# Kernel tuning notes

Hardware: AMD Instinct MI355X
Metric: run time of the kernel (lower is better)

Reference implementation:

```python
import jax, jax.numpy as jnp
import numpy as np

B, S, D, H = 2, 2048, 1024, 16
DK = D // H


def setup_inputs() -> dict:
    key = jax.random.key(0)
    ks = jax.random.split(key, 9)
    sc = 0.02
    return {
        "x": jax.random.normal(ks[0], (B, S, D), dtype=jnp.float32),
        "attention_mask": jnp.ones((B, S), dtype=jnp.int32),
        "Wq": jax.random.normal(ks[1], (D, D), dtype=jnp.float32) * sc,
        "bq": jax.random.normal(ks[2], (D,), dtype=jnp.float32) * sc,
        "Wk": jax.random.normal(ks[3], (D, D), dtype=jnp.float32) * sc,
        "bk": jax.random.normal(ks[4], (D,), dtype=jnp.float32) * sc,
        "Wv": jax.random.normal(ks[5], (D, D), dtype=jnp.float32) * sc,
        "bv": jax.random.normal(ks[6], (D,), dtype=jnp.float32) * sc,
        "Wo": jax.random.normal(ks[7], (D, D), dtype=jnp.float32) * sc,
        "bo": jax.random.normal(ks[8], (D,), dtype=jnp.float32) * sc,
    }


def reference(x, attention_mask, Wq, bq, Wk, bk, Wv, bv, Wo, bo):
    b, s, d = x.shape
    # projections (Linear: x @ W + b) then split heads -> [b, h, s, dk]
    def heads(t):
        return t.reshape(b, s, H, DK).transpose(0, 2, 1, 3)
    Q = heads(x @ Wq + bq)
    K = heads(x @ Wk + bk)
    V = heads(x @ Wv + bv)
    # NOTE: original computes K @ Q^T (not Q @ K^T) and applies NO 1/sqrt(dk) scale
    scores = jnp.einsum("bhid,bhjd->bhij", K, Q)  # [b, h, s, s]
    causal = jnp.tril(jnp.ones((s, s), dtype=bool))  # [s, s]
    final_mask = attention_mask[:, None, None, :].astype(bool) & causal[None, None]
    scores = jnp.where(final_mask, scores, -jnp.inf)
    attn = jax.nn.softmax(scores, axis=-1)
    out = jnp.einsum("bhij,bhjd->bhid", attn, V)  # [b, h, s, dk]
    out = out.transpose(0, 2, 1, 3).reshape(b, s, d)
    return out @ Wo + bo
```

## Files before the change

### kernel.cpp

```cpp
#include <hip/hip_runtime.h>
#include <stdint.h>
#include <stddef.h>


typedef short bf16x8 __attribute__((ext_vector_type(8)));
typedef float f32x4  __attribute__((ext_vector_type(4)));

__device__ __forceinline__ short f2bf(float f) {
  union { float f; uint32_t u; } a; a.f = f;
  uint32_t r = a.u + 0x7fffu + ((a.u >> 16) & 1u);
  return (short)(r >> 16);
}
__device__ __forceinline__ float bf2f(short s) {
  union { uint32_t u; float f; } a; a.u = ((uint32_t)(uint16_t)s) << 16;
  return a.f;
}
__device__ __forceinline__ uint32_t pack2bf(float a, float b) {
  union { float f; uint32_t u; } x, y; x.f = a; y.f = b;
  return (x.u >> 16) | (y.u & 0xffff0000u);
}
__device__ __forceinline__ float fast_exp2(float x) {
#if __has_builtin(__builtin_amdgcn_exp2f)
  return __builtin_amdgcn_exp2f(x);
#else
  return exp2f(x);
#endif
}
__device__ __forceinline__ void async16(const void* g, void* l) {
  __builtin_amdgcn_global_load_lds(
      (const __attribute__((address_space(1))) uint32_t*)g,
      (__attribute__((address_space(3))) uint32_t*)l, 16, 0, 0);
}
#define MFMA(a, b, c) __builtin_amdgcn_mfma_f32_16x16x32_bf16((a), (b), (c), 0, 0, 0)

__global__ void k_split_x(const float* __restrict__ x, short* __restrict__ xhi,
                          short* __restrict__ xlo) {
  int i = blockIdx.x * 256 + threadIdx.x;
  float4 v = ((const float4*)x)[i];
  short4 h, l;
  h.x = f2bf(v.x); l.x = f2bf(v.x - bf2f(h.x));
  h.y = f2bf(v.y); l.y = f2bf(v.y - bf2f(h.y));
  h.z = f2bf(v.z); l.z = f2bf(v.z - bf2f(h.z));
  h.w = f2bf(v.w); l.w = f2bf(v.w - bf2f(h.w));
  ((short4*)xhi)[i] = h;
  ((short4*)xlo)[i] = l;
}

__global__ void k_prep_w(const float* __restrict__ Wq, const float* __restrict__ Wk,
                         const float* __restrict__ Wv, const float* __restrict__ Wo,
                         short* __restrict__ whi, short* __restrict__ wo) {
  __shared__ float T[64][65];
  int z = blockIdx.z;
  const float* W = (z == 0) ? Wq : (z == 1) ? Wk : (z == 2) ? Wv : Wo;
  int n0 = blockIdx.x * 64, k0 = blockIdx.y * 64;
  int t = threadIdx.x;
  int rr = t >> 4, cc = (t & 15) * 4;
#pragma unroll
  for (int it = 0; it < 4; ++it) {
    int row = rr + it * 16;
    float4 v = *(const float4*)&W[(size_t)(k0 + row) * 1024 + n0 + cc];
    T[row][cc] = v.x; T[row][cc + 1] = v.y; T[row][cc + 2] = v.z; T[row][cc + 3] = v.w;
  }
  __syncthreads();
  short* oh = (z < 3) ? (whi + (size_t)z * 1048576) : wo;
#pragma unroll
  for (int it = 0; it < 4; ++it) {
    int nrow = rr + it * 16;
    short4 h4;
    h4.x = f2bf(T[cc + 0][nrow]);
    h4.y = f2bf(T[cc + 1][nrow]);
    h4.z = f2bf(T[cc + 2][nrow]);
    h4.w = f2bf(T[cc + 3][nrow]);
    *(short4*)&oh[(size_t)(n0 + nrow) * 1024 + k0 + cc] = h4;
  }
}

__global__ __launch_bounds__(256, 3) void k_gemm_qkv(
    const short* __restrict__ xhi, const short* __restrict__ xlo,
    const short* __restrict__ whi,
    const float* __restrict__ bq, const float* __restrict__ bk,
    const float* __restrict__ bv,
    short* __restrict__ Qhi, short* __restrict__ Qlo,
    short* __restrict__ Khi, short* __restrict__ Klo,
    short* __restrict__ Vt) {
  __shared__ short AH[2][4096];
  __shared__ short AL[2][4096];
  __shared__ short BH[2][4096];
  int tid = threadIdx.x;
  int bx = blockIdx.x;
  int m0 = blockIdx.y * 128;
  int n0g = bx * 128;
  bool SPLIT = (bx < 16);
  int w = tid >> 6, lane = tid & 63, lr = lane & 15, lq = lane >> 4;
  int wm = w >> 1, wn = w & 1;
  f32x4 acc[4][4] = {};

  auto stage = [&](int ks, int pb) {
#pragma unroll
    for (int it = 0; it < 2; ++it) {
      int idx = it * 256 + tid;
      int row = idx >> 2, c = idx & 3;
      int cs = c ^ (row & 3);
      size_t ga = (size_t)(m0 + row) * 1024 + ks * 32 + cs * 8;
      async16(xhi + ga, &AH[pb][idx * 8]);
      if (SPLIT) async16(xlo + ga, &AL[pb][idx * 8]);
      size_t gb = (size_t)(n0g + row) * 1024 + ks * 32 + cs * 8;
      async16(whi + gb, &BH[pb][idx * 8]);
    }
  };

  stage(0, 0);
  int p = 0;
  int g = lq ^ (lr & 3);
  for (int ks = 0; ks < 32; ++ks) {
    __syncthreads();
    if (ks < 31) stage(ks + 1, p ^ 1);
    const bf16x8* A8 = (const bf16x8*)AH[p];
    const bf16x8* L8 = (const bf16x8*)AL[p];
    const bf16x8* B8 = (const bf16x8*)BH[p];
    bf16x8 af[4], al[4], bfr[4];
#pragma unroll
    for (int mt = 0; mt < 4; ++mt) af[mt] = A8[(wm * 64 + mt * 16 + lr) * 4 + g];
#pragma unroll
    for (int nt = 0; nt < 4; ++nt) bfr[nt] = B8[(wn * 64 + nt * 16 + lr) * 4 + g];
    if (SPLIT) {
#pragma unroll
      for (int mt = 0; mt < 4; ++mt) al[mt] = L8[(wm * 64 + mt * 16 + lr) * 4 + g];
    }
#pragma unroll
    for (int mt = 0; mt < 4; ++mt)
#pragma unroll
      for (int nt = 0; nt < 4; ++nt)
        acc[mt][nt] = MFMA(af[mt], bfr[nt], acc[mt][nt]);
    if (SPLIT) {
#pragma unroll
      for (int mt = 0; mt < 4; ++mt)
#pragma unroll
        for (int nt = 0; nt < 4; ++nt)
          acc[mt][nt] = MFMA(al[mt], bfr[nt], acc[mt][nt]);
    }
    p ^= 1;
  }

  int z = bx >> 3;
  const float LOG2E = 1.44269504f;
  if (z == 2) {
#pragma unroll
    for (int nt = 0; nt < 4; ++nt) {
      int dg = (n0g & 1023) + wn * 64 + nt * 16 + lr;
      float bvv = bv[dg];
      int hh = dg >> 6, dk = dg & 63;
#pragma unroll
      for (int mt = 0; mt < 4; ++mt) {
        int row = m0 + wm * 64 + mt * 16 + lq * 4;
        int b_ = row >> 11, s_ = row & 2047;
        short4 pk;
        pk.x = f2bf(acc[mt][nt][0] + bvv);
        pk.y = f2bf(acc[mt][nt][1] + bvv);
        pk.z = f2bf(acc[mt][nt][2] + bvv);
        pk.w = f2bf(acc[mt][nt][3] + bvv);
        *(short4*)&Vt[(size_t)((b_ * 16 + hh) * 64 + dk) * 2048 + s_] = pk;
      }
    }
  } else {
    const float* bias = (z == 0) ? bq : bk;
    short* Ch = (z == 0) ? Qhi : Khi;
    short* Cl = (z == 0) ? Qlo : Klo;
#pragma unroll
    for (int nt = 0; nt < 4; ++nt) {
      int colg = (n0g & 1023) + wn * 64 + nt * 16 + lr;
      float bvv = bias[colg];
#pragma unroll
      for (int mt = 0; mt < 4; ++mt)
#pragma unroll
        for (int r = 0; r < 4; ++r) {
          int row = m0 + wm * 64 + mt * 16 + lq * 4 + r;
          float v = acc[mt][nt][r] + bvv;
          if (z == 0) v *= LOG2E;
          size_t o = (size_t)row * 1024 + colg;
          short hh = f2bf(v);
          Ch[o] = hh;
          Cl[o] = f2bf(v - bf2f(hh));
        }
    }
  }
}

__global__ __launch_bounds__(256, 2) void k_gemm_o(
    const short* __restrict__ Ab, const short* __restrict__ Bb,
    const float* __restrict__ bias, float* __restrict__ Cf) {
  __shared__ short AH[2][4096];
  __shared__ short BH[2][4096];
  int tid = threadIdx.x;
  int m0 = blockIdx.y * 128, n0 = blockIdx.x * 128;
  int w = tid >> 6, lane = tid & 63, lr = lane & 15, lq = lane >> 4;
  int wm = w >> 1, wn = w & 1;
  f32x4 acc[4][4] = {};

  auto stage = [&](int ks, int pb) {
#pragma unroll
    for (int it = 0; it < 2; ++it) {
      int idx = it * 256 + tid;
      int row = idx >> 2, c = idx & 3;
      int cs = c ^ (row & 3);
      async16(Ab + (size_t)(m0 + row) * 1024 + ks * 32 + cs * 8, &AH[pb][idx * 8]);
      async16(Bb + (size_t)(n0 + row) * 1024 + ks * 32 + cs * 8, &BH[pb][idx * 8]);
    }
  };

  stage(0, 0);
  int p = 0;
  int g = lq ^ (lr & 3);
  for (int ks = 0; ks < 32; ++ks) {
    __syncthreads();
    if (ks < 31) stage(ks + 1, p ^ 1);
    const bf16x8* A8 = (const bf16x8*)AH[p];
    const bf16x8* B8 = (const bf16x8*)BH[p];
    bf16x8 af[4], bfr[4];
#pragma unroll
    for (int mt = 0; mt < 4; ++mt) af[mt] = A8[(wm * 64 + mt * 16 + lr) * 4 + g];
#pragma unroll
    for (int nt = 0; nt < 4; ++nt) bfr[nt] = B8[(wn * 64 + nt * 16 + lr) * 4 + g];
#pragma unroll
    for (int mt = 0; mt < 4; ++mt)
#pragma unroll
      for (int nt = 0; nt < 4; ++nt)
        acc[mt][nt] = MFMA(af[mt], bfr[nt], acc[mt][nt]);
    p ^= 1;
  }
#pragma unroll
  for (int nt = 0; nt < 4; ++nt) {
    int col = n0 + wn * 64 + nt * 16 + lr;
    float bvv = bias[col];
#pragma unroll
    for (int mt = 0; mt < 4; ++mt)
#pragma unroll
      for (int r = 0; r < 4; ++r) {
        int row = m0 + wm * 64 + mt * 16 + lq * 4 + r;
        Cf[(size_t)row * 1024 + col] = acc[mt][nt][r] + bvv;
      }
  }
}

__global__ __launch_bounds__(128, 2) void k_attn(
    const short* __restrict__ Khi, const short* __restrict__ Klo,
    const short* __restrict__ Qhi, const short* __restrict__ Qlo,
    const short* __restrict__ Vt, const int* __restrict__ amask,
    short* __restrict__ Obuf) {
  __shared__ short QH[4096];
  __shared__ short QL[4096];
  __shared__ short VS[4096];
  int tid = threadIdx.x;
  int bid = blockIdx.x;
  int xcd = bid & 7, slot = bid >> 3;
  int bh = xcd * 4 + (slot >> 5);
  int p  = slot & 31;
  int b = bh >> 4, h = bh & 15;
  int w = tid >> 6, lane = tid & 63, lr = lane & 15, lq = lane >> 4;
  int bandA = p, bandB = 63 - p;
  int nA = ((p * 32 + 31) >> 6) + 1;

  f32x4 OA[4] = {}, OB[4] = {};
  float lsA = 0.f, lsB = 0.f;
  int baddr0 = (((lq & 1) * 2) * 16 + lr) * 4;
  int baddr1 = baddr0 + 64;

  bf16x8 kh[2], kl[2];
  const bf16x8* Q8 = (const bf16x8*)QH;
  const bf16x8* L8 = (const bf16x8*)QL;
  const bf16x8* V8 = (const bf16x8*)VS;

  for (int t = 0; t < 33; ++t) {
    bool isA = (t < nA);
    int band = isA ? bandA : bandB;
    int jt = isA ? t : t - nA;
    int j0 = jt * 64;
#pragma unroll
    for (int it = 0; it < 4; ++it) {
      int idx = it * 128 + tid;
      int rr = idx >> 3, c = idx & 7;
      int cs = c ^ (rr & 7);
      size_t gq = ((size_t)(b * 2048 + j0 + rr)) * 1024 + h * 64 + cs * 8;
      async16(Qhi + gq, &QH[idx * 8]);
      async16(Qlo + gq, &QL[idx * 8]);
      size_t gv = ((size_t)(bh * 64 + rr)) * 2048 + j0 + cs * 8;
      async16(Vt + gv, &VS[idx * 8]);
    }
    if (t == 0 || t == nA) {
      size_t ra = ((size_t)(b * 2048 + band * 32 + w * 16 + lr)) * 1024 + h * 64;
#pragma unroll
      for (int ks = 0; ks < 2; ++ks) {
        kh[ks] = *(const bf16x8*)(Khi + ra + ks * 32 + lq * 8);
        kl[ks] = *(const bf16x8*)(Klo + ra + ks * 32 + lq * 8);
      }
    }
    __syncthreads();

    int av = amask[b * 2048 + j0 + lane];
    unsigned long long bal = __ballot(av != 0);
    bool allv = (bal == ~0ull);

    f32x4 s[4] = {};
#pragma unroll
    for (int mt = 0; mt < 4; ++mt) {
      int row = mt * 16 + lr;
#pragma unroll
      for (int ks = 0; ks < 2; ++ks) {
        int gi = row * 8 + ((ks * 4 + lq) ^ (row & 7));
        bf16x8 qa = Q8[gi];
        bf16x8 la = L8[gi];
        s[mt] = MFMA(qa, kh[ks], s[mt]);
        s[mt] = MFMA(la, kh[ks], s[mt]);
        s[mt] = MFMA(qa, kl[ks], s[mt]);
      }
    }

    bool diag = (t == nA - 1) || (t == 32);
    int iq = band * 32 + w * 16 + lr;
    float pv[4][4];
#pragma unroll
    for (int mt = 0; mt < 4; ++mt)
#pragma unroll
      for (int r = 0; r < 4; ++r)
        pv[mt][r] = fast_exp2(s[mt][r]);
    if (diag) {
#pragma unroll
      for (int mt = 0; mt < 4; ++mt)
#pragma unroll
        for (int r = 0; r < 4; ++r)
          if (j0 + mt * 16 + lq * 4 + r > iq) pv[mt][r] = 0.f;
    }
    if (!allv) {
#pragma unroll
      for (int mt = 0; mt < 4; ++mt)
#pragma unroll
        for (int r = 0; r < 4; ++r)
          if (!((bal >> (mt * 16 + lq * 4 + r)) & 1)) pv[mt][r] = 0.f;
    }
    uint32_t pd[4][2];
    float lt = 0.f;
#pragma unroll
    for (int mt = 0; mt < 4; ++mt) {
      lt += (pv[mt][0] + pv[mt][1]) + (pv[mt][2] + pv[mt][3]);
      pd[mt][0] = pack2bf(pv[mt][0], pv[mt][1]);
      pd[mt][1] = pack2bf(pv[mt][2], pv[mt][3]);
    }
    if (isA) lsA += lt; else lsB += lt;

    f32x4* O = isA ? OA : OB;
#pragma unroll
    for (int k2 = 0; k2 < 2; ++k2) {
      union { int i[4]; bf16x8 v; } pa;
#pragma unroll
      for (int dd = 0; dd < 4; ++dd) {
        int addr = (dd >> 1) ? baddr1 : baddr0;
        int v0 = __builtin_amdgcn_ds_bpermute(addr, (int)pd[k2 * 2 + 0][dd & 1]);
        int v1 = __builtin_amdgcn_ds_bpermute(addr, (int)pd[k2 * 2 + 1][dd & 1]);
        pa.i[dd] = (lq >> 1) ? v1 : v0;
      }
#pragma unroll
      for (int nt = 0; nt < 4; ++nt) {
        int row = nt * 16 + lr;
        bf16x8 vb = V8[row * 8 + ((k2 * 4 + lq) ^ (row & 7))];
        O[nt] = MFMA(pa.v, vb, O[nt]);
      }
    }
    __syncthreads();
  }

  auto fin = [&](f32x4* O, float ls, int band) {
    float tsum = ls;
    tsum += __shfl_xor(tsum, 16);
    tsum += __shfl_xor(tsum, 32);
    float inv[4];
#pragma unroll
    for (int r = 0; r < 4; ++r) inv[r] = 1.0f / __shfl(tsum, lq * 4 + r, 64);
#pragma unroll
    for (int nt = 0; nt < 4; ++nt)
#pragma unroll
      for (int r = 0; r < 4; ++r) {
        int row = b * 2048 + band * 32 + w * 16 + lq * 4 + r;
        int col = h * 64 + nt * 16 + lr;
        Obuf[(size_t)row * 1024 + col] = f2bf(O[nt][r] * inv[r]);
      }
  };
  fin(OA, lsA, bandA);
  fin(OB, lsB, bandB);
}

extern "C" void kernel_launch(void* const* d_in, const int* in_sizes, int n_in,
                              void* d_out, int out_size, void* d_ws, size_t ws_size,
                              hipStream_t stream) {
  const float* x  = (const float*)d_in[0];
  const int* amask = (const int*)d_in[1];
  const float* Wq = (const float*)d_in[2];
  const float* bq = (const float*)d_in[3];
  const float* Wk = (const float*)d_in[4];
  const float* bk = (const float*)d_in[5];
  const float* Wv = (const float*)d_in[6];
  const float* bv = (const float*)d_in[7];
  const float* Wo = (const float*)d_in[8];
  const float* bo = (const float*)d_in[9];

  char* ws = (char*)d_ws;
  const size_t MB = 1024 * 1024;
  short* xhi = (short*)(ws);
  short* xlo = (short*)(ws + 8 * MB);
  short* whi = (short*)(ws + 16 * MB);
  short* wo  = (short*)(ws + 26 * MB);
  short* Qhi = (short*)(ws + 28 * MB);
  short* Qlo = (short*)(ws + 36 * MB);
  short* Khi = (short*)(ws + 44 * MB);
  short* Klo = (short*)(ws + 52 * MB);
  short* Vt  = (short*)(ws + 60 * MB);
  short* Obuf = xhi;

  k_split_x<<<4096, 256, 0, stream>>>(x, xhi, xlo);
  k_prep_w<<<dim3(16, 16, 4), 256, 0, stream>>>(Wq, Wk, Wv, Wo, whi, wo);

  k_gemm_qkv<<<dim3(24, 32), 256, 0, stream>>>(xhi, xlo, whi, bq, bk, bv,
                                               Qhi, Qlo, Khi, Klo, Vt);
  k_attn<<<1024, 128, 0, stream>>>(Khi, Klo, Qhi, Qlo, Vt, amask, Obuf);
  k_gemm_o<<<dim3(8, 32), 256, 0, stream>>>(Obuf, wo, bo, (float*)d_out);
}
```

Before: 241.7 us.

## Double-buffer attention tiles, 4-warp band pairs, and halve output GEMM tile width

The attention kernel now uses 256 threads, so each block owns two adjacent 32-row query bands, and it double-buffers the Q/V tiles in shared memory. The next tile's async load is issued while the current one is being computed, and one barrier per iteration is dropped. The old pairing of a short band with a long band (33 iterations per block) is replaced by variable-length blocks ordered longest first, which relies on the scheduler to balance the work. The output GEMM switches to 128x64 tiles with more blocks and higher occupancy. In exchange, shared memory per attention block doubles and the work is spread unevenly across blocks.

```diff
diff --git a/kernel.cpp b/kernel.cpp
--- a/kernel.cpp
+++ b/kernel.cpp
@@ -186,16 +186,15 @@
   }
 }
 
-__global__ __launch_bounds__(256, 2) void k_gemm_o(
+__global__ __launch_bounds__(256, 4) void k_gemm_o(
     const short* __restrict__ Ab, const short* __restrict__ Bb,
     const float* __restrict__ bias, float* __restrict__ Cf) {
   __shared__ short AH[2][4096];
-  __shared__ short BH[2][4096];
+  __shared__ short BH[2][2048];
   int tid = threadIdx.x;
-  int m0 = blockIdx.y * 128, n0 = blockIdx.x * 128;
+  int m0 = blockIdx.y * 128, n0 = blockIdx.x * 64;
   int w = tid >> 6, lane = tid & 63, lr = lane & 15, lq = lane >> 4;
-  int wm = w >> 1, wn = w & 1;
-  f32x4 acc[4][4] = {};
+  f32x4 acc[2][4] = {};
 
   auto stage = [&](int ks, int pb) {
 #pragma unroll
@@ -204,6 +203,11 @@
       int row = idx >> 2, c = idx & 3;
       int cs = c ^ (row & 3);
       async16(Ab + (size_t)(m0 + row) * 1024 + ks * 32 + cs * 8, &AH[pb][idx * 8]);
+    }
+    {
+      int idx = tid;
+      int row = idx >> 2, c = idx & 3;
+      int cs = c ^ (row & 3);
       async16(Bb + (size_t)(n0 + row) * 1024 + ks * 32 + cs * 8, &BH[pb][idx * 8]);
     }
   };
@@ -216,13 +220,13 @@
     if (ks < 31) stage(ks + 1, p ^ 1);
     const bf16x8* A8 = (const bf16x8*)AH[p];
     const bf16x8* B8 = (const bf16x8*)BH[p];
-    bf16x8 af[4], bfr[4];
-#pragma unroll
-    for (int mt = 0; mt < 4; ++mt) af[mt] = A8[(wm * 64 + mt * 16 + lr) * 4 + g];
-#pragma unroll
-    for (int nt = 0; nt < 4; ++nt) bfr[nt] = B8[(wn * 64 + nt * 16 + lr) * 4 + g];
-#pragma unroll
-    for (int mt = 0; mt < 4; ++mt)
+    bf16x8 af[2], bfr[4];
+#pragma unroll
+    for (int mt = 0; mt < 2; ++mt) af[mt] = A8[(w * 32 + mt * 16 + lr) * 4 + g];
+#pragma unroll
+    for (int nt = 0; nt < 4; ++nt) bfr[nt] = B8[(nt * 16 + lr) * 4 + g];
+#pragma unroll
+    for (int mt = 0; mt < 2; ++mt)
 #pragma unroll
       for (int nt = 0; nt < 4; ++nt)
         acc[mt][nt] = MFMA(af[mt], bfr[nt], acc[mt][nt]);
@@ -230,71 +234,76 @@
   }
 #pragma unroll
   for (int nt = 0; nt < 4; ++nt) {
-    int col = n0 + wn * 64 + nt * 16 + lr;
+    int col = n0 + nt * 16 + lr;
     float bvv = bias[col];
 #pragma unroll
-    for (int mt = 0; mt < 4; ++mt)
+    for (int mt = 0; mt < 2; ++mt)
 #pragma unroll
       for (int r = 0; r < 4; ++r) {
-        int row = m0 + wm * 64 + mt * 16 + lq * 4 + r;
+        int row = m0 + w * 32 + mt * 16 + lq * 4 + r;
         Cf[(size_t)row * 1024 + col] = acc[mt][nt][r] + bvv;
       }
   }
 }
 
-__global__ __launch_bounds__(128, 2) void k_attn(
+__global__ __launch_bounds__(256, 3) void k_attn(
     const short* __restrict__ Khi, const short* __restrict__ Klo,
     const short* __restrict__ Qhi, const short* __restrict__ Qlo,
     const short* __restrict__ Vt, const int* __restrict__ amask,
     short* __restrict__ Obuf) {
-  __shared__ short QH[4096];
-  __shared__ short QL[4096];
-  __shared__ short VS[4096];
+  __shared__ short QH[2][4096];
+  __shared__ short QL[2][4096];
+  __shared__ short VS[2][4096];
   int tid = threadIdx.x;
   int bid = blockIdx.x;
-  int xcd = bid & 7, slot = bid >> 3;
-  int bh = xcd * 4 + (slot >> 5);
-  int p  = slot & 31;
+  int xcd = bid & 7, idx = bid >> 3;
+  int bh = xcd * 4 + (idx >> 5);
+  int L  = 32 - (idx & 31);
   int b = bh >> 4, h = bh & 15;
   int w = tid >> 6, lane = tid & 63, lr = lane & 15, lq = lane >> 4;
-  int bandA = p, bandB = 63 - p;
-  int nA = ((p * 32 + 31) >> 6) + 1;
-
-  f32x4 OA[4] = {}, OB[4] = {};
-  float lsA = 0.f, lsB = 0.f;
+  int band = 2 * (L - 1) + (w >> 1);
+  int rb0 = band * 32 + (w & 1) * 16;
+
+  bf16x8 kh[2], kl[2];
+  {
+    size_t ra = ((size_t)(b * 2048 + rb0 + lr)) * 1024 + h * 64;
+#pragma unroll
+    for (int ks = 0; ks < 2; ++ks) {
+      kh[ks] = *(const bf16x8*)(Khi + ra + ks * 32 + lq * 8);
+      kl[ks] = *(const bf16x8*)(Klo + ra + ks * 32 + lq * 8);
+    }
+  }
+
+  f32x4 O[4] = {};
+  float ls = 0.f;
+  int iq = rb0 + lr;
   int baddr0 = (((lq & 1) * 2) * 16 + lr) * 4;
   int baddr1 = baddr0 + 64;
 
-  bf16x8 kh[2], kl[2];
-  const bf16x8* Q8 = (const bf16x8*)QH;
-  const bf16x8* L8 = (const bf16x8*)QL;
-  const bf16x8* V8 = (const bf16x8*)VS;
-
-  for (int t = 0; t < 33; ++t) {
-    bool isA = (t < nA);
-    int band = isA ? bandA : bandB;
-    int jt = isA ? t : t - nA;
+  auto stage = [&](int jt, int pb) {
     int j0 = jt * 64;
 #pragma unroll
-    for (int it = 0; it < 4; ++it) {
-      int idx = it * 128 + tid;
-      int rr = idx >> 3, c = idx & 7;
+    for (int it = 0; it < 2; ++it) {
+      int idx2 = it * 256 + tid;
+      int rr = idx2 >> 3, c = idx2 & 7;
       int cs = c ^ (rr & 7);
       size_t gq = ((size_t)(b * 2048 + j0 + rr)) * 1024 + h * 64 + cs * 8;
-      async16(Qhi + gq, &QH[idx * 8]);
-      async16(Qlo + gq, &QL[idx * 8]);
+      async16(Qhi + gq, &QH[pb][idx2 * 8]);
+      async16(Qlo + gq, &QL[pb][idx2 * 8]);
       size_t gv = ((size_t)(bh * 64 + rr)) * 2048 + j0 + cs * 8;
-      async16(Vt + gv, &VS[idx * 8]);
-    }
-    if (t == 0 || t == nA) {
-      size_t ra = ((size_t)(b * 2048 + band * 32 + w * 16 + lr)) * 1024 + h * 64;
-#pragma unroll
-      for (int ks = 0; ks < 2; ++ks) {
-        kh[ks] = *(const bf16x8*)(Khi + ra + ks * 32 + lq * 8);
-        kl[ks] = *(const bf16x8*)(Klo + ra + ks * 32 + lq * 8);
-      }
-    }
+      async16(Vt + gv, &VS[pb][idx2 * 8]);
+    }
+  };
+
+  stage(0, 0);
+  int p = 0;
+  for (int t = 0; t < L; ++t) {
     __syncthreads();
+    if (t + 1 < L) stage(t + 1, p ^ 1);
+    int j0 = t * 64;
+    const bf16x8* Q8 = (const bf16x8*)QH[p];
+    const bf16x8* L8 = (const bf16x8*)QL[p];
+    const bf16x8* V8 = (const bf16x8*)VS[p];
 
     int av = amask[b * 2048 + j0 + lane];
     unsigned long long bal = __ballot(av != 0);
@@ -315,8 +324,7 @@
       }
     }
 
-    bool diag = (t == nA - 1) || (t == 32);
-    int iq = band * 32 + w * 16 + lr;
+    bool diag = (t == L - 1);
     float pv[4][4];
 #pragma unroll
     for (int mt = 0; mt < 4; ++mt)
@@ -338,16 +346,13 @@
           if (!((bal >> (mt * 16 + lq * 4 + r)) & 1)) pv[mt][r] = 0.f;
     }
     uint32_t pd[4][2];
-    float lt = 0.f;
 #pragma unroll
     for (int mt = 0; mt < 4; ++mt) {
-      lt += (pv[mt][0] + pv[mt][1]) + (pv[mt][2] + pv[mt][3]);
+      ls += (pv[mt][0] + pv[mt][1]) + (pv[mt][2] + pv[mt][3]);
       pd[mt][0] = pack2bf(pv[mt][0], pv[mt][1]);
       pd[mt][1] = pack2bf(pv[mt][2], pv[mt][3]);
     }
-    if (isA) lsA += lt; else lsB += lt;
-
-    f32x4* O = isA ? OA : OB;
+
 #pragma unroll
     for (int k2 = 0; k2 < 2; ++k2) {
       union { int i[4]; bf16x8 v; } pa;
@@ -365,27 +370,23 @@
         O[nt] = MFMA(pa.v, vb, O[nt]);
       }
     }
-    __syncthreads();
-  }
-
-  auto fin = [&](f32x4* O, float ls, int band) {
-    float tsum = ls;
-    tsum += __shfl_xor(tsum, 16);
-    tsum += __shfl_xor(tsum, 32);
-    float inv[4];
-#pragma unroll
-    for (int r = 0; r < 4; ++r) inv[r] = 1.0f / __shfl(tsum, lq * 4 + r, 64);
-#pragma unroll
-    for (int nt = 0; nt < 4; ++nt)
-#pragma unroll
-      for (int r = 0; r < 4; ++r) {
-        int row = b * 2048 + band * 32 + w * 16 + lq * 4 + r;
-        int col = h * 64 + nt * 16 + lr;
-        Obuf[(size_t)row * 1024 + col] = f2bf(O[nt][r] * inv[r]);
-      }
-  };
-  fin(OA, lsA, bandA);
-  fin(OB, lsB, bandB);
+    p ^= 1;
+  }
+
+  float tsum = ls;
+  tsum += __shfl_xor(tsum, 16);
+  tsum += __shfl_xor(tsum, 32);
+  float inv[4];
+#pragma unroll
+  for (int r = 0; r < 4; ++r) inv[r] = 1.0f / __shfl(tsum, lq * 4 + r, 64);
+#pragma unroll
+  for (int nt = 0; nt < 4; ++nt)
+#pragma unroll
+    for (int r = 0; r < 4; ++r) {
+      int row = b * 2048 + rb0 + lq * 4 + r;
+      int col = h * 64 + nt * 16 + lr;
+      Obuf[(size_t)row * 1024 + col] = f2bf(O[nt][r] * inv[r]);
+    }
 }
 
 extern "C" void kernel_launch(void* const* d_in, const int* in_sizes, int n_in,
@@ -420,6 +421,6 @@
 
   k_gemm_qkv<<<dim3(24, 32), 256, 0, stream>>>(xhi, xlo, whi, bq, bk, bv,
                                                Qhi, Qlo, Khi, Klo, Vt);
-  k_attn<<<1024, 128, 0, stream>>>(Khi, Klo, Qhi, Qlo, Vt, amask, Obuf);
-  k_gemm_o<<<dim3(8, 32), 256, 0, stream>>>(Obuf, wo, bo, (float*)d_out);
-}
+  k_attn<<<1024, 256, 0, stream>>>(Khi, Klo, Qhi, Qlo, Vt, amask, Obuf);
+  k_gemm_o<<<dim3(16, 32), 256, 0, stream>>>(Obuf, wo, bo, (float*)d_out);
+}
```

Result: no change. 239.4 us (-0.9%).
